# Optimization experiments

Hardware: AMD Instinct MI355X
Metric: run time of the kernel (lower is better)

The kernel has to match this reference:

```python
import jax, jax.numpy as jnp
import numpy as np

N_TOKENS = 8192
D_MODEL = 1024
D_HIDDEN = 4096
N_EXPERTS = 8
TOP_K = 2


def setup_inputs() -> dict:
    key = jax.random.key(0)
    ks = jax.random.split(key, 7)
    s = 0.02
    return {
        "x": jax.random.normal(ks[0], (N_TOKENS, D_MODEL), dtype=jnp.float32),
        "gate_w": jax.random.normal(ks[1], (D_MODEL, N_EXPERTS), dtype=jnp.float32) * s,
        "gate_b": jnp.zeros((N_EXPERTS,), dtype=jnp.float32),
        "w1": jax.random.normal(ks[2], (N_EXPERTS, D_MODEL, D_HIDDEN), dtype=jnp.float32) * s,
        "b1": jnp.zeros((N_EXPERTS, D_HIDDEN), dtype=jnp.float32),
        "w2": jax.random.normal(ks[3], (N_EXPERTS, D_HIDDEN, D_MODEL), dtype=jnp.float32) * s,
        "b2": jnp.zeros((N_EXPERTS, D_MODEL), dtype=jnp.float32),
    }


def reference(x, gate_w, gate_b, w1, b1, w2, b2):
    # Gating: softmax over experts, then top-k routing
    gate_scores = jax.nn.softmax(x @ gate_w + gate_b, axis=-1)        # [N, E]
    topk_vals, topk_idx = jax.lax.top_k(gate_scores, TOP_K)          # [N, K]

    # Combine weights: sum of topk_vals scattered to expert slots
    onehot = jax.nn.one_hot(topk_idx, N_EXPERTS, dtype=x.dtype)      # [N, K, E]
    combine = jnp.einsum('nk,nke->ne', topk_vals, onehot)            # [N, E]

    # Dense expert evaluation (math identical to masked dispatch: unselected
    # experts receive weight 0 in `combine`).
    h = jax.nn.relu(jnp.einsum('nd,edh->neh', x, w1) + b1)           # [N, E, H]
    expert_out = jnp.einsum('neh,ehd->ned', h, w2) + b2              # [N, E, D]
    output = jnp.einsum('ned,ne->nd', expert_out, combine)           # [N, D]

    # Load-balancing loss from routing counts
    load = jnp.sum(onehot, axis=(0, 1))                              # [E]
    load_balancing_loss = jnp.sum((load / jnp.sum(load)) ** 2)
    return output, load_balancing_loss
```

## Files before the change

### kernel.cpp

```cpp
#include <hip/hip_runtime.h>

#define D_MODEL   1024
#define D_HIDDEN  4096
#define N_EXPERTS 8
#define N_TOKENS  8192
#define NASSIGN   (N_TOKENS * 2)
#define PADCAP    (NASSIGN + N_EXPERTS * 128)
#define ROWT      (PADCAP / 128)

typedef unsigned short u16;
typedef __bf16 bf16x8 __attribute__((ext_vector_type(8)));
typedef float  f32x4  __attribute__((ext_vector_type(4)));

__device__ __forceinline__ u16 f2bf(float f) {
  union { float f; unsigned u; } c; c.f = f;
  unsigned u = c.u;
  u = (u + 0x7fffu + ((u >> 16) & 1u)) >> 16;
  return (u16)u;
}

__device__ __forceinline__ void async16(const void* g, void* l) {
  __builtin_amdgcn_global_load_lds(
      (const __attribute__((address_space(1))) unsigned int*)g,
      (__attribute__((address_space(3))) unsigned int*)l, 16, 0, 0);
}

__global__ __launch_bounds__(64) void gating_kernel(
    const float* __restrict__ x, const float* __restrict__ gw,
    const float* __restrict__ gb, int* __restrict__ counts,
    int* __restrict__ tok_idx, float* __restrict__ tok_w)
{
  const int n = blockIdx.x;
  const int lane = threadIdx.x;
  float acc[8] = {0.f,0.f,0.f,0.f,0.f,0.f,0.f,0.f};
  for (int d = lane; d < D_MODEL; d += 64) {
    float xv = x[(size_t)n * D_MODEL + d];
    const float4* g = (const float4*)&gw[d * 8];
    float4 g0 = g[0], g1 = g[1];
    acc[0] += xv * g0.x; acc[1] += xv * g0.y; acc[2] += xv * g0.z; acc[3] += xv * g0.w;
    acc[4] += xv * g1.x; acc[5] += xv * g1.y; acc[6] += xv * g1.z; acc[7] += xv * g1.w;
  }
  for (int off = 32; off; off >>= 1)
    #pragma unroll
    for (int e = 0; e < 8; ++e) acc[e] += __shfl_xor(acc[e], off, 64);
  if (lane == 0) {
    float l[8], p[8];
    float m = -1e30f;
    for (int e = 0; e < 8; ++e) { l[e] = acc[e] + gb[e]; m = fmaxf(m, l[e]); }
    float s = 0.f;
    for (int e = 0; e < 8; ++e) { p[e] = expf(l[e] - m); s += p[e]; }
    float inv = 1.f / s;
    for (int e = 0; e < 8; ++e) p[e] *= inv;
    int i0 = 0;
    for (int e = 1; e < 8; ++e) if (p[e] > p[i0]) i0 = e;
    int i1 = (i0 == 0) ? 1 : 0;
    for (int e = 0; e < 8; ++e) if (e != i0 && p[e] > p[i1]) i1 = e;
    tok_idx[2 * n]     = i0;  tok_idx[2 * n + 1] = i1;
    tok_w[2 * n]       = p[i0]; tok_w[2 * n + 1] = p[i1];
    atomicAdd(&counts[i0], 1);
    atomicAdd(&counts[i1], 1);
  }
}

__global__ void finalize_routing(const int* __restrict__ counts,
                                 int* __restrict__ offsets,
                                 float* __restrict__ out_loss)
{
  int off = 0;
  for (int e = 0; e < 8; ++e) {
    offsets[e] = off;
    off += ((counts[e] + 127) >> 7) << 7;
  }
  offsets[8] = off;
  float loss = 0.f;
  for (int e = 0; e < 8; ++e) {
    float f = (float)counts[e] * (1.f / (float)NASSIGN);
    loss += f * f;
  }
  *out_loss = loss;
}

__global__ __launch_bounds__(256) void scatter_kernel(
    const int* __restrict__ tok_idx, const float* __restrict__ tok_w,
    const int* __restrict__ offsets, int* __restrict__ cursors,
    int* __restrict__ assign_token, float* __restrict__ assign_w)
{
  const int n = blockIdx.x * 256 + threadIdx.x;
  #pragma unroll
  for (int k = 0; k < 2; ++k) {
    int e = tok_idx[n * 2 + k];
    int pos = offsets[e] + atomicAdd(&cursors[e], 1);
    assign_token[pos] = n;
    assign_w[pos] = tok_w[n * 2 + k];
  }
}

__global__ __launch_bounds__(256) void convert_x_kernel(
    const float* __restrict__ x, u16* __restrict__ xb)
{
  size_t i = ((size_t)blockIdx.x * 256 + threadIdx.x) * 4;
  float4 v = *(const float4*)&x[i];
  unsigned lo = (unsigned)f2bf(v.x) | ((unsigned)f2bf(v.y) << 16);
  unsigned hi = (unsigned)f2bf(v.z) | ((unsigned)f2bf(v.w) << 16);
  uint2 o; o.x = lo; o.y = hi;
  *(uint2*)&xb[i] = o;
}

__global__ __launch_bounds__(256) void transpose_cvt_kernel(
    const float* __restrict__ in, u16* __restrict__ out, int R, int C)
{
  const int e = blockIdx.z;
  const int c0 = blockIdx.x * 32, r0 = blockIdx.y * 32;
  __shared__ float tile[32][33];
  const int tx = threadIdx.x & 31, ty = threadIdx.x >> 5;
  const float* ip = in + (size_t)e * R * C;
  u16* op = out + (size_t)e * R * C;
  #pragma unroll
  for (int i = 0; i < 4; ++i)
    tile[ty + i * 8][tx] = ip[(size_t)(r0 + ty + i * 8) * C + c0 + tx];
  __syncthreads();
  #pragma unroll
  for (int i = 0; i < 4; ++i)
    op[(size_t)(c0 + ty + i * 8) * R + r0 + tx] = f2bf(tile[tx][ty + i * 8]);
}

__global__ __launch_bounds__(256) void gemm1_kernel(
    const u16* __restrict__ xb, const u16* __restrict__ w1t,
    const float* __restrict__ b1, const int* __restrict__ assign_token,
    const int* __restrict__ offsets, u16* __restrict__ hbuf)
{
  const int rt = blockIdx.x, ct = blockIdx.y;
  if (rt * 128 >= offsets[8]) return;
  int e = 0;
  while (offsets[e + 1] <= rt * 128) ++e;

  __shared__ __align__(16) u16 As[128 * 32];
  __shared__ __align__(16) u16 Bs[128 * 32];
  __shared__ __align__(16) u16 Hs[128 * 128];

  const int tid = threadIdx.x;
  const int wave = tid >> 6, lane = tid & 63;

  const int c0 = tid, c1 = tid + 256;
  const int r0 = c0 >> 2, s0 = c0 & 3;
  const int r1 = c1 >> 2, s1 = c1 & 3;
  const int sg0 = s0 ^ ((r0 >> 1) & 3);
  const int sg1 = s1 ^ ((r1 >> 1) & 3);

  const long aBase0 = (long)assign_token[rt * 128 + r0] * D_MODEL + sg0 * 8;
  const long aBase1 = (long)assign_token[rt * 128 + r1] * D_MODEL + sg1 * 8;
  const long bBase0 = ((long)e * D_HIDDEN + ct * 128 + r0) * D_MODEL + sg0 * 8;
  const long bBase1 = ((long)e * D_HIDDEN + ct * 128 + r1) * D_MODEL + sg1 * 8;

  u16* ldsA0 = &As[(wave * 64) * 8];
  u16* ldsA1 = &As[(256 + wave * 64) * 8];
  u16* ldsB0 = &Bs[(wave * 64) * 8];
  u16* ldsB1 = &Bs[(256 + wave * 64) * 8];

  const int wr = (wave >> 1) * 64, wc = (wave & 1) * 64;
  f32x4 acc[4][4];
  #pragma unroll
  for (int i = 0; i < 4; ++i)
    #pragma unroll
    for (int j = 0; j < 4; ++j) acc[i][j] = (f32x4){0.f, 0.f, 0.f, 0.f};

  int aoff[4], boff[4];
  #pragma unroll
  for (int i = 0; i < 4; ++i) {
    int row = wr + i * 16 + (lane & 15);
    aoff[i] = row * 32 + (((lane >> 4) ^ ((row >> 1) & 3)) * 8);
    int rown = wc + i * 16 + (lane & 15);
    boff[i] = rown * 32 + (((lane >> 4) ^ ((rown >> 1) & 3)) * 8);
  }

  for (int k0 = 0; k0 < D_MODEL; k0 += 32) {
    __syncthreads();
    async16(xb + aBase0 + k0, ldsA0);
    async16(xb + aBase1 + k0, ldsA1);
    async16(w1t + bBase0 + k0, ldsB0);
    async16(w1t + bBase1 + k0, ldsB1);
    __syncthreads();
    bf16x8 a[4], b[4];
    #pragma unroll
    for (int i = 0; i < 4; ++i) a[i] = *(const bf16x8*)&As[aoff[i]];
    #pragma unroll
    for (int j = 0; j < 4; ++j) b[j] = *(const bf16x8*)&Bs[boff[j]];
    #pragma unroll
    for (int i = 0; i < 4; ++i)
      #pragma unroll
      for (int j = 0; j < 4; ++j)
        acc[i][j] = __builtin_amdgcn_mfma_f32_16x16x32_bf16(a[i], b[j], acc[i][j], 0, 0, 0);
  }

  float bias[4];
  #pragma unroll
  for (int j = 0; j < 4; ++j)
    bias[j] = b1[(size_t)e * D_HIDDEN + ct * 128 + wc + j * 16 + (lane & 15)];

  #pragma unroll
  for (int i = 0; i < 4; ++i)
    #pragma unroll
    for (int j = 0; j < 4; ++j)
      #pragma unroll
      for (int r = 0; r < 4; ++r) {
        int rl = wr + i * 16 + ((lane >> 4) * 4) + r;
        int cl = wc + j * 16 + (lane & 15);
        Hs[rl * 128 + cl] = f2bf(fmaxf(acc[i][j][r] + bias[j], 0.f));
      }
  __syncthreads();
  #pragma unroll
  for (int t = 0; t < 8; ++t) {
    int cc = tid + t * 256;
    int row = cc >> 4, cs = cc & 15;
    *(uint4*)&hbuf[((size_t)(rt * 128 + row)) * D_HIDDEN + ct * 128 + cs * 8] =
        *(const uint4*)&Hs[row * 128 + cs * 8];
  }
}

__global__ __launch_bounds__(256) void gemm2_kernel(
    const u16* __restrict__ hbuf, const u16* __restrict__ w2t,
    const float* __restrict__ b2, const int* __restrict__ assign_token,
    const float* __restrict__ assign_w, const int* __restrict__ offsets,
    float* __restrict__ out)
{
  const int rt = blockIdx.x, ct = blockIdx.y;
  if (rt * 128 >= offsets[8]) return;
  int e = 0;
  while (offsets[e + 1] <= rt * 128) ++e;

  __shared__ __align__(16) u16 As[128 * 32];
  __shared__ __align__(16) u16 Bs[128 * 32];
  __shared__ int tokS[128];
  __shared__ float wS[128];

  const int tid = threadIdx.x;
  const int wave = tid >> 6, lane = tid & 63;
  if (tid < 128) {
    tokS[tid] = assign_token[rt * 128 + tid];
    wS[tid] = assign_w[rt * 128 + tid];
  }

  const int c0 = tid, c1 = tid + 256;
  const int r0 = c0 >> 2, s0 = c0 & 3;
  const int r1 = c1 >> 2, s1 = c1 & 3;
  const int sg0 = s0 ^ ((r0 >> 1) & 3);
  const int sg1 = s1 ^ ((r1 >> 1) & 3);

  const long aBase0 = ((long)(rt * 128 + r0)) * D_HIDDEN + sg0 * 8;
  const long aBase1 = ((long)(rt * 128 + r1)) * D_HIDDEN + sg1 * 8;
  const long bBase0 = ((long)e * D_MODEL + ct * 128 + r0) * D_HIDDEN + sg0 * 8;
  const long bBase1 = ((long)e * D_MODEL + ct * 128 + r1) * D_HIDDEN + sg1 * 8;

  u16* ldsA0 = &As[(wave * 64) * 8];
  u16* ldsA1 = &As[(256 + wave * 64) * 8];
  u16* ldsB0 = &Bs[(wave * 64) * 8];
  u16* ldsB1 = &Bs[(256 + wave * 64) * 8];

  const int wr = (wave >> 1) * 64, wc = (wave & 1) * 64;
  f32x4 acc[4][4];
  #pragma unroll
  for (int i = 0; i < 4; ++i)
    #pragma unroll
    for (int j = 0; j < 4; ++j) acc[i][j] = (f32x4){0.f, 0.f, 0.f, 0.f};

  int aoff[4], boff[4];
  #pragma unroll
  for (int i = 0; i < 4; ++i) {
    int row = wr + i * 16 + (lane & 15);
    aoff[i] = row * 32 + (((lane >> 4) ^ ((row >> 1) & 3)) * 8);
    int rown = wc + i * 16 + (lane & 15);
    boff[i] = rown * 32 + (((lane >> 4) ^ ((rown >> 1) & 3)) * 8);
  }

  for (int k0 = 0; k0 < D_HIDDEN; k0 += 32) {
    __syncthreads();
    async16(hbuf + aBase0 + k0, ldsA0);
    async16(hbuf + aBase1 + k0, ldsA1);
    async16(w2t + bBase0 + k0, ldsB0);
    async16(w2t + bBase1 + k0, ldsB1);
    __syncthreads();
    bf16x8 a[4], b[4];
    #pragma unroll
    for (int i = 0; i < 4; ++i) a[i] = *(const bf16x8*)&As[aoff[i]];
    #pragma unroll
    for (int j = 0; j < 4; ++j) b[j] = *(const bf16x8*)&Bs[boff[j]];
    #pragma unroll
    for (int i = 0; i < 4; ++i)
      #pragma unroll
      for (int j = 0; j < 4; ++j)
        acc[i][j] = __builtin_amdgcn_mfma_f32_16x16x32_bf16(a[i], b[j], acc[i][j], 0, 0, 0);
  }

  float bias[4];
  #pragma unroll
  for (int j = 0; j < 4; ++j)
    bias[j] = b2[(size_t)e * D_MODEL + ct * 128 + wc + j * 16 + (lane & 15)];

  #pragma unroll
  for (int i = 0; i < 4; ++i)
    #pragma unroll
    for (int r = 0; r < 4; ++r) {
      int rl = wr + i * 16 + ((lane >> 4) * 4) + r;
      int tok = tokS[rl];
      float wgt = wS[rl];
      #pragma unroll
      for (int j = 0; j < 4; ++j) {
        float v = (acc[i][j][r] + bias[j]) * wgt;
        atomicAdd(&out[(size_t)tok * D_MODEL + ct * 128 + wc + j * 16 + (lane & 15)], v);
      }
    }
}

__global__ __launch_bounds__(256) void moe_fallback_kernel(
    const float* __restrict__ x, const float* __restrict__ w1,
    const float* __restrict__ b1, const float* __restrict__ w2,
    const float* __restrict__ b2, const int* __restrict__ tok_idx,
    const float* __restrict__ tok_w, float* __restrict__ out)
{
  const int a = blockIdx.x;
  const int n = a >> 1, slot = a & 1;
  const int e = tok_idx[n * 2 + slot];
  const float wgt = tok_w[n * 2 + slot];
  __shared__ float xs[D_MODEL];
  __shared__ float hs[D_HIDDEN];
  const int tid = threadIdx.x;
  for (int d = tid; d < D_MODEL; d += 256) xs[d] = x[(size_t)n * D_MODEL + d];
  __syncthreads();
  for (int h = tid; h < D_HIDDEN; h += 256) {
    float acc = b1[(size_t)e * D_HIDDEN + h];
    for (int d = 0; d < D_MODEL; ++d)
      acc += xs[d] * w1[((size_t)e * D_MODEL + d) * D_HIDDEN + h];
    hs[h] = fmaxf(acc, 0.f);
  }
  __syncthreads();
  for (int d = tid; d < D_MODEL; d += 256) {
    float acc = b2[(size_t)e * D_MODEL + d];
    for (int h = 0; h < D_HIDDEN; ++h)
      acc += hs[h] * w2[((size_t)e * D_HIDDEN + h) * D_MODEL + d];
    atomicAdd(&out[(size_t)n * D_MODEL + d], wgt * acc);
  }
}

extern "C" void kernel_launch(void* const* d_in, const int* in_sizes, int n_in,
                              void* d_out, int out_size, void* d_ws, size_t ws_size,
                              hipStream_t stream) {
  const float* x      = (const float*)d_in[0];
  const float* gate_w = (const float*)d_in[1];
  const float* gate_b = (const float*)d_in[2];
  const float* w1     = (const float*)d_in[3];
  const float* b1     = (const float*)d_in[4];
  const float* w2     = (const float*)d_in[5];
  const float* b2     = (const float*)d_in[6];
  float* out = (float*)d_out;

  char* ws = (char*)d_ws;
  int*   counts       = (int*)(ws + 0);
  int*   cursors      = (int*)(ws + 32);
  int*   offsets      = (int*)(ws + 64);
  int*   tok_idx      = (int*)(ws + 256);
  float* tok_w        = (float*)(ws + 256 + 65536);
  int*   assign_token = (int*)(ws + 131328);
  float* assign_w     = (float*)(ws + 200960);
  const size_t X0 = 274432;
  u16* xb   = (u16*)(ws + X0);
  u16* w1t  = (u16*)(ws + X0 + 16777216);
  u16* w2t  = (u16*)(ws + X0);
  u16* hbuf = (u16*)(ws + X0 + 83886080);
  const size_t REQ = X0 + 83886080ull + 142606336ull;

  hipMemsetAsync(d_out, 0, (size_t)out_size * sizeof(float), stream);

  const bool fast = (ws_size >= REQ);
  hipMemsetAsync(ws, 0, fast ? 270592 : 131328, stream);

  gating_kernel<<<N_TOKENS, 64, 0, stream>>>(x, gate_w, gate_b, counts, tok_idx, tok_w);
  finalize_routing<<<1, 1, 0, stream>>>(counts, offsets, out + (out_size - 1));

  if (fast) {
    scatter_kernel<<<N_TOKENS / 256, 256, 0, stream>>>(tok_idx, tok_w, offsets, cursors,
                                                       assign_token, assign_w);
    convert_x_kernel<<<(N_TOKENS * D_MODEL) / 1024, 256, 0, stream>>>(x, xb);
    transpose_cvt_kernel<<<dim3(D_HIDDEN / 32, D_MODEL / 32, N_EXPERTS), 256, 0, stream>>>(
        w1, w1t, D_MODEL, D_HIDDEN);
    gemm1_kernel<<<dim3(ROWT, D_HIDDEN / 128), 256, 0, stream>>>(
        xb, w1t, b1, assign_token, offsets, hbuf);
    transpose_cvt_kernel<<<dim3(D_MODEL / 32, D_HIDDEN / 32, N_EXPERTS), 256, 0, stream>>>(
        w2, w2t, D_HIDDEN, D_MODEL);
    gemm2_kernel<<<dim3(ROWT, D_MODEL / 128), 256, 0, stream>>>(
        hbuf, w2t, b2, assign_token, assign_w, offsets, out);
  } else {
    moe_fallback_kernel<<<NASSIGN, 256, 0, stream>>>(x, w1, b1, w2, b2, tok_idx, tok_w, out);
  }
}
```

Measured before the change: 895.6 us.

## Double-buffer GEMM K-tiles and replace atomic scatter with gather combine

Both expert GEMMs now use two LDS stages so the next K-tile's async loads overlap the current tile's MFMA work, with one barrier per iteration instead of two. When enough workspace is available, GEMM2 writes weighted per-assignment outputs to a buffer and a new combine kernel sums each token's two rows, replacing global fp32 atomicAdds and the output memset. This adds an extra write and read of a large fp32 buffer and requires more workspace, falling back to the atomic path otherwise.

```diff
diff --git a/kernel.cpp b/kernel.cpp
--- a/kernel.cpp
+++ b/kernel.cpp
@@ -83,7 +83,8 @@
 __global__ __launch_bounds__(256) void scatter_kernel(
     const int* __restrict__ tok_idx, const float* __restrict__ tok_w,
     const int* __restrict__ offsets, int* __restrict__ cursors,
-    int* __restrict__ assign_token, float* __restrict__ assign_w)
+    int* __restrict__ assign_token, float* __restrict__ assign_w,
+    int* __restrict__ tok_pos)
 {
   const int n = blockIdx.x * 256 + threadIdx.x;
   #pragma unroll
@@ -92,6 +93,7 @@
     int pos = offsets[e] + atomicAdd(&cursors[e], 1);
     assign_token[pos] = n;
     assign_w[pos] = tok_w[n * 2 + k];
+    tok_pos[n * 2 + k] = pos;
   }
 }
 
@@ -134,9 +136,7 @@
   int e = 0;
   while (offsets[e + 1] <= rt * 128) ++e;
 
-  __shared__ __align__(16) u16 As[128 * 32];
-  __shared__ __align__(16) u16 Bs[128 * 32];
-  __shared__ __align__(16) u16 Hs[128 * 128];
+  __shared__ __align__(16) u16 smem[16384];
 
   const int tid = threadIdx.x;
   const int wave = tid >> 6, lane = tid & 63;
@@ -152,11 +152,6 @@
   const long bBase0 = ((long)e * D_HIDDEN + ct * 128 + r0) * D_MODEL + sg0 * 8;
   const long bBase1 = ((long)e * D_HIDDEN + ct * 128 + r1) * D_MODEL + sg1 * 8;
 
-  u16* ldsA0 = &As[(wave * 64) * 8];
-  u16* ldsA1 = &As[(256 + wave * 64) * 8];
-  u16* ldsB0 = &Bs[(wave * 64) * 8];
-  u16* ldsB1 = &Bs[(256 + wave * 64) * 8];
-
   const int wr = (wave >> 1) * 64, wc = (wave & 1) * 64;
   f32x4 acc[4][4];
   #pragma unroll
@@ -173,30 +168,43 @@
     boff[i] = rown * 32 + (((lane >> 4) ^ ((rown >> 1) & 3)) * 8);
   }
 
-  for (int k0 = 0; k0 < D_MODEL; k0 += 32) {
-    __syncthreads();
-    async16(xb + aBase0 + k0, ldsA0);
-    async16(xb + aBase1 + k0, ldsA1);
-    async16(w1t + bBase0 + k0, ldsB0);
-    async16(w1t + bBase1 + k0, ldsB1);
-    __syncthreads();
+  #define STAGE1(p, k0) do { \
+    u16* A_ = smem + (p) * 4096; \
+    u16* B_ = smem + 8192 + (p) * 4096; \
+    async16(xb  + aBase0 + (k0), A_ + wave * 512); \
+    async16(xb  + aBase1 + (k0), A_ + 2048 + wave * 512); \
+    async16(w1t + bBase0 + (k0), B_ + wave * 512); \
+    async16(w1t + bBase1 + (k0), B_ + 2048 + wave * 512); \
+  } while (0)
+
+  STAGE1(0, 0);
+  __syncthreads();
+  int p = 0;
+  for (int t = 0; t < D_MODEL / 32; ++t) {
+    if (t < D_MODEL / 32 - 1) STAGE1(p ^ 1, (t + 1) * 32);
+    const u16* A = smem + p * 4096;
+    const u16* B = smem + 8192 + p * 4096;
     bf16x8 a[4], b[4];
     #pragma unroll
-    for (int i = 0; i < 4; ++i) a[i] = *(const bf16x8*)&As[aoff[i]];
-    #pragma unroll
-    for (int j = 0; j < 4; ++j) b[j] = *(const bf16x8*)&Bs[boff[j]];
+    for (int i = 0; i < 4; ++i) a[i] = *(const bf16x8*)&A[aoff[i]];
+    #pragma unroll
+    for (int j = 0; j < 4; ++j) b[j] = *(const bf16x8*)&B[boff[j]];
     #pragma unroll
     for (int i = 0; i < 4; ++i)
       #pragma unroll
       for (int j = 0; j < 4; ++j)
         acc[i][j] = __builtin_amdgcn_mfma_f32_16x16x32_bf16(a[i], b[j], acc[i][j], 0, 0, 0);
-  }
+    __syncthreads();
+    p ^= 1;
+  }
+  #undef STAGE1
 
   float bias[4];
   #pragma unroll
   for (int j = 0; j < 4; ++j)
     bias[j] = b1[(size_t)e * D_HIDDEN + ct * 128 + wc + j * 16 + (lane & 15)];
 
+  u16* Hs = smem;
   #pragma unroll
   for (int i = 0; i < 4; ++i)
     #pragma unroll
@@ -217,19 +225,19 @@
   }
 }
 
+template <bool EO>
 __global__ __launch_bounds__(256) void gemm2_kernel(
     const u16* __restrict__ hbuf, const u16* __restrict__ w2t,
     const float* __restrict__ b2, const int* __restrict__ assign_token,
     const float* __restrict__ assign_w, const int* __restrict__ offsets,
-    float* __restrict__ out)
+    float* __restrict__ dst)
 {
   const int rt = blockIdx.x, ct = blockIdx.y;
   if (rt * 128 >= offsets[8]) return;
   int e = 0;
   while (offsets[e + 1] <= rt * 128) ++e;
 
-  __shared__ __align__(16) u16 As[128 * 32];
-  __shared__ __align__(16) u16 Bs[128 * 32];
+  __shared__ __align__(16) u16 smem[16384];
   __shared__ int tokS[128];
   __shared__ float wS[128];
 
@@ -251,11 +259,6 @@
   const long bBase0 = ((long)e * D_MODEL + ct * 128 + r0) * D_HIDDEN + sg0 * 8;
   const long bBase1 = ((long)e * D_MODEL + ct * 128 + r1) * D_HIDDEN + sg1 * 8;
 
-  u16* ldsA0 = &As[(wave * 64) * 8];
-  u16* ldsA1 = &As[(256 + wave * 64) * 8];
-  u16* ldsB0 = &Bs[(wave * 64) * 8];
-  u16* ldsB1 = &Bs[(256 + wave * 64) * 8];
-
   const int wr = (wave >> 1) * 64, wc = (wave & 1) * 64;
   f32x4 acc[4][4];
   #pragma unroll
@@ -272,24 +275,36 @@
     boff[i] = rown * 32 + (((lane >> 4) ^ ((rown >> 1) & 3)) * 8);
   }
 
-  for (int k0 = 0; k0 < D_HIDDEN; k0 += 32) {
-    __syncthreads();
-    async16(hbuf + aBase0 + k0, ldsA0);
-    async16(hbuf + aBase1 + k0, ldsA1);
-    async16(w2t + bBase0 + k0, ldsB0);
-    async16(w2t + bBase1 + k0, ldsB1);
-    __syncthreads();
+  #define STAGE2(p, k0) do { \
+    u16* A_ = smem + (p) * 4096; \
+    u16* B_ = smem + 8192 + (p) * 4096; \
+    async16(hbuf + aBase0 + (k0), A_ + wave * 512); \
+    async16(hbuf + aBase1 + (k0), A_ + 2048 + wave * 512); \
+    async16(w2t  + bBase0 + (k0), B_ + wave * 512); \
+    async16(w2t  + bBase1 + (k0), B_ + 2048 + wave * 512); \
+  } while (0)
+
+  STAGE2(0, 0);
+  __syncthreads();
+  int p = 0;
+  for (int t = 0; t < D_HIDDEN / 32; ++t) {
+    if (t < D_HIDDEN / 32 - 1) STAGE2(p ^ 1, (t + 1) * 32);
+    const u16* A = smem + p * 4096;
+    const u16* B = smem + 8192 + p * 4096;
     bf16x8 a[4], b[4];
     #pragma unroll
-    for (int i = 0; i < 4; ++i) a[i] = *(const bf16x8*)&As[aoff[i]];
-    #pragma unroll
-    for (int j = 0; j < 4; ++j) b[j] = *(const bf16x8*)&Bs[boff[j]];
+    for (int i = 0; i < 4; ++i) a[i] = *(const bf16x8*)&A[aoff[i]];
+    #pragma unroll
+    for (int j = 0; j < 4; ++j) b[j] = *(const bf16x8*)&B[boff[j]];
     #pragma unroll
     for (int i = 0; i < 4; ++i)
       #pragma unroll
       for (int j = 0; j < 4; ++j)
         acc[i][j] = __builtin_amdgcn_mfma_f32_16x16x32_bf16(a[i], b[j], acc[i][j], 0, 0, 0);
-  }
+    __syncthreads();
+    p ^= 1;
+  }
+  #undef STAGE2
 
   float bias[4];
   #pragma unroll
@@ -301,14 +316,37 @@
     #pragma unroll
     for (int r = 0; r < 4; ++r) {
       int rl = wr + i * 16 + ((lane >> 4) * 4) + r;
-      int tok = tokS[rl];
       float wgt = wS[rl];
-      #pragma unroll
-      for (int j = 0; j < 4; ++j) {
-        float v = (acc[i][j][r] + bias[j]) * wgt;
-        atomicAdd(&out[(size_t)tok * D_MODEL + ct * 128 + wc + j * 16 + (lane & 15)], v);
+      if (EO) {
+        size_t row = (size_t)(rt * 128 + rl);
+        #pragma unroll
+        for (int j = 0; j < 4; ++j) {
+          float v = (acc[i][j][r] + bias[j]) * wgt;
+          dst[row * D_MODEL + ct * 128 + wc + j * 16 + (lane & 15)] = v;
+        }
+      } else {
+        int tok = tokS[rl];
+        #pragma unroll
+        for (int j = 0; j < 4; ++j) {
+          float v = (acc[i][j][r] + bias[j]) * wgt;
+          atomicAdd(&dst[(size_t)tok * D_MODEL + ct * 128 + wc + j * 16 + (lane & 15)], v);
+        }
       }
     }
+}
+
+__global__ __launch_bounds__(256) void combine_kernel(
+    const float* __restrict__ eo, const int* __restrict__ tok_pos,
+    float* __restrict__ out)
+{
+  int idx = blockIdx.x * 256 + threadIdx.x;
+  int n = idx >> 8;
+  int c = (idx & 255) * 4;
+  int p0 = tok_pos[2 * n], p1 = tok_pos[2 * n + 1];
+  float4 a = *(const float4*)&eo[(size_t)p0 * D_MODEL + c];
+  float4 b = *(const float4*)&eo[(size_t)p1 * D_MODEL + c];
+  float4 o; o.x = a.x + b.x; o.y = a.y + b.y; o.z = a.z + b.z; o.w = a.w + b.w;
+  *(float4*)&out[(size_t)n * D_MODEL + c] = o;
 }
 
 __global__ __launch_bounds__(256) void moe_fallback_kernel(
@@ -358,27 +396,33 @@
   int*   cursors      = (int*)(ws + 32);
   int*   offsets      = (int*)(ws + 64);
   int*   tok_idx      = (int*)(ws + 256);
-  float* tok_w        = (float*)(ws + 256 + 65536);
-  int*   assign_token = (int*)(ws + 131328);
-  float* assign_w     = (float*)(ws + 200960);
-  const size_t X0 = 274432;
+  float* tok_w        = (float*)(ws + 65792);
+  int*   tok_pos      = (int*)(ws + 131328);
+  int*   assign_token = (int*)(ws + 196864);
+  float* assign_w     = (float*)(ws + 266496);
+  const size_t X0 = 336128;
   u16* xb   = (u16*)(ws + X0);
   u16* w1t  = (u16*)(ws + X0 + 16777216);
   u16* w2t  = (u16*)(ws + X0);
   u16* hbuf = (u16*)(ws + X0 + 83886080);
-  const size_t REQ = X0 + 83886080ull + 142606336ull;
-
-  hipMemsetAsync(d_out, 0, (size_t)out_size * sizeof(float), stream);
-
-  const bool fast = (ws_size >= REQ);
-  hipMemsetAsync(ws, 0, fast ? 270592 : 131328, stream);
+  float* eo = (float*)(ws + X0 + 226492416ull);
+  const size_t REQ_FAST = X0 + 226492416ull;
+  const size_t REQ_EO   = REQ_FAST + 71303168ull;
+
+  const bool fast = (ws_size >= REQ_FAST);
+  const bool eoPath = (ws_size >= REQ_EO);
+
+  hipMemsetAsync(ws, 0, fast ? X0 : 336128, stream);
+  if (!eoPath) {
+    hipMemsetAsync(d_out, 0, (size_t)out_size * sizeof(float), stream);
+  }
 
   gating_kernel<<<N_TOKENS, 64, 0, stream>>>(x, gate_w, gate_b, counts, tok_idx, tok_w);
   finalize_routing<<<1, 1, 0, stream>>>(counts, offsets, out + (out_size - 1));
 
   if (fast) {
     scatter_kernel<<<N_TOKENS / 256, 256, 0, stream>>>(tok_idx, tok_w, offsets, cursors,
-                                                       assign_token, assign_w);
+                                                       assign_token, assign_w, tok_pos);
     convert_x_kernel<<<(N_TOKENS * D_MODEL) / 1024, 256, 0, stream>>>(x, xb);
     transpose_cvt_kernel<<<dim3(D_HIDDEN / 32, D_MODEL / 32, N_EXPERTS), 256, 0, stream>>>(
         w1, w1t, D_MODEL, D_HIDDEN);
@@ -386,8 +430,14 @@
         xb, w1t, b1, assign_token, offsets, hbuf);
     transpose_cvt_kernel<<<dim3(D_MODEL / 32, D_HIDDEN / 32, N_EXPERTS), 256, 0, stream>>>(
         w2, w2t, D_HIDDEN, D_MODEL);
-    gemm2_kernel<<<dim3(ROWT, D_MODEL / 128), 256, 0, stream>>>(
-        hbuf, w2t, b2, assign_token, assign_w, offsets, out);
+    if (eoPath) {
+      gemm2_kernel<true><<<dim3(ROWT, D_MODEL / 128), 256, 0, stream>>>(
+          hbuf, w2t, b2, assign_token, assign_w, offsets, eo);
+      combine_kernel<<<(N_TOKENS * D_MODEL) / 1024, 256, 0, stream>>>(eo, tok_pos, out);
+    } else {
+      gemm2_kernel<false><<<dim3(ROWT, D_MODEL / 128), 256, 0, stream>>>(
+          hbuf, w2t, b2, assign_token, assign_w, offsets, out);
+    }
   } else {
     moe_fallback_kernel<<<NASSIGN, 256, 0, stream>>>(x, w1, b1, w2, b2, tok_idx, tok_w, out);
   }
```

New measurement: 831.3 us. -7.2%, faster.
